# Kernel tuning notes

Measured on AMD Instinct MI355X. Metric: run time of the kernel, lower is better.

## Reference

```python
import jax, jax.numpy as jnp
import numpy as np

EMBED_DIM = 1280
NUM_HEADS = 20
HEAD_DIM = EMBED_DIM // NUM_HEADS
SEQ = 1024
BSZ = 8
ROPE_BASE = 10000.0


def _rope_cos_sin(seq_len, dim, dtype):
    # ESM RotaryEmbedding: inv_freq over even indices, emb = concat(freqs, freqs)
    inv_freq = 1.0 / (ROPE_BASE ** (jnp.arange(0, dim, 2, dtype=jnp.float32) / dim))
    t = jnp.arange(seq_len, dtype=jnp.float32)
    freqs = t[:, None] * inv_freq[None, :]          # [S, D/2]
    emb = jnp.concatenate([freqs, freqs], axis=-1)  # [S, D]
    return jnp.cos(emb).astype(dtype), jnp.sin(emb).astype(dtype)


def _rotate_half(x):
    x1, x2 = jnp.split(x, 2, axis=-1)
    return jnp.concatenate([-x2, x1], axis=-1)


def _apply_rotary(x, cos, sin):
    # x: [B, H, S, D]; cos/sin: [S, D] broadcast over B, H
    return x * cos[None, None, :, :] + _rotate_half(x) * sin[None, None, :, :]


def setup_inputs() -> dict:
    key = jax.random.key(0)
    ks = jax.random.split(key, 9)
    s = 0.02
    return {
        "query": jax.random.normal(ks[0], (SEQ, BSZ, EMBED_DIM), jnp.float32),
        "q_w": jax.random.normal(ks[1], (EMBED_DIM, EMBED_DIM), jnp.float32) * s,
        "q_b": jax.random.normal(ks[2], (EMBED_DIM,), jnp.float32) * s,
        "k_w": jax.random.normal(ks[3], (EMBED_DIM, EMBED_DIM), jnp.float32) * s,
        "k_b": jax.random.normal(ks[4], (EMBED_DIM,), jnp.float32) * s,
        "v_w": jax.random.normal(ks[5], (EMBED_DIM, EMBED_DIM), jnp.float32) * s,
        "v_b": jax.random.normal(ks[6], (EMBED_DIM,), jnp.float32) * s,
        "out_w": jax.random.normal(ks[7], (EMBED_DIM, EMBED_DIM), jnp.float32) * s,
        "out_b": jax.random.normal(ks[8], (EMBED_DIM,), jnp.float32) * s,
    }


def reference(query, q_w, q_b, k_w, k_b, v_w, v_b, out_w, out_b):
    T, B, E = query.shape
    H, D = NUM_HEADS, HEAD_DIM
    scaling = D ** -0.5

    # Separate Q/K/V projections (self-attention: key = value = query)
    q = query @ q_w.T + q_b
    k = query @ k_w.T + k_b
    v = query @ v_w.T + v_b

    # [T, B, E] -> [B, H, T, D]
    def split_heads(x):
        return x.reshape(T, B, H, D).transpose(1, 2, 0, 3)

    q, k, v = split_heads(q), split_heads(k), split_heads(v)

    # Rotary embeddings on q, k
    cos, sin = _rope_cos_sin(T, D, q.dtype)
    q = _apply_rotary(q, cos, sin)
    k = _apply_rotary(k, cos, sin)

    # SDPA with explicit scale = head_dim^-0.5
    scores = jnp.einsum("bhtd,bhsd->bhts", q, k) * scaling
    probs = jax.nn.softmax(scores, axis=-1)
    attn = jnp.einsum("bhts,bhsd->bhtd", probs, v)  # [B, H, T, D]

    # [B, H, T, D] -> [T, B, E]
    attn = attn.transpose(2, 0, 1, 3).reshape(T, B, E)
    return attn @ out_w.T + out_b
```

## Files before the change

### kernel.cpp

```cpp
#include <hip/hip_runtime.h>
#include <math.h>

#define T_SEQ 1024
#define BSZ   8
#define EMB   1280
#define NH    20
#define HD    64
#define MROWS 8192
#define KBYTES (EMB * 2)

typedef __attribute__((ext_vector_type(8))) short bf16x8;
typedef __attribute__((ext_vector_type(4))) float f32x4;

__device__ __forceinline__ short f2bf(float f) {
    unsigned u = __float_as_uint(f);
    u += 0x7fff + ((u >> 16) & 1);
    return (short)(u >> 16);
}
__device__ __forceinline__ float bf2f(short s) {
    return __uint_as_float(((unsigned)(unsigned short)s) << 16);
}

__device__ __forceinline__ void gld16(const void* g, void* l) {
    __builtin_amdgcn_global_load_lds(
        (const __attribute__((address_space(1))) void*)g,
        (__attribute__((address_space(3))) void*)l, 16, 0, 0);
}

__global__ __launch_bounds__(256) void f2bf_kernel(
    const float* __restrict__ in, short* __restrict__ out, int n8)
{
    int i = blockIdx.x * 256 + threadIdx.x;
    if (i >= n8) return;
    const float4* p = (const float4*)in;
    float4 x = p[2 * i], y = p[2 * i + 1];
    bf16x8 o;
    o[0] = f2bf(x.x); o[1] = f2bf(x.y); o[2] = f2bf(x.z); o[3] = f2bf(x.w);
    o[4] = f2bf(y.x); o[5] = f2bf(y.y); o[6] = f2bf(y.z); o[7] = f2bf(y.w);
    ((bf16x8*)out)[i] = o;
}

__global__ __launch_bounds__(256) void wcast_kernel(
    const float* __restrict__ w0, const float* __restrict__ w1,
    const float* __restrict__ w2, const float* __restrict__ w3,
    short* __restrict__ o0, short* __restrict__ o1,
    short* __restrict__ o2, short* __restrict__ o3, int n8)
{
    int which = blockIdx.y;
    const float* in = (which == 0) ? w0 : (which == 1) ? w1 : (which == 2) ? w2 : w3;
    short* out      = (which == 0) ? o0 : (which == 1) ? o1 : (which == 2) ? o2 : o3;
    int i = blockIdx.x * 256 + threadIdx.x;
    if (i >= n8) return;
    const float4* p = (const float4*)in;
    float4 x = p[2 * i], y = p[2 * i + 1];
    bf16x8 o;
    o[0] = f2bf(x.x); o[1] = f2bf(x.y); o[2] = f2bf(x.z); o[3] = f2bf(x.w);
    o[4] = f2bf(y.x); o[5] = f2bf(y.y); o[6] = f2bf(y.z); o[7] = f2bf(y.w);
    ((bf16x8*)out)[i] = o;
}

__global__ void rope_table_kernel(float* __restrict__ cost, float* __restrict__ sint) {
    int idx = blockIdx.x * 256 + threadIdx.x;
    if (idx >= T_SEQ * 32) return;
    int i = idx & 31, t = idx >> 5;
    float inv = powf(10000.0f, -(float)i / 32.0f);
    float f = (float)t * inv;
    cost[idx] = cosf(f);
    sint[idx] = sinf(f);
}

__device__ __forceinline__ void gemm_core(
    const short* __restrict__ A, const short* __restrict__ B,
    char* As, char* Bs, int m0, int n0, int tid, f32x4 (&acc)[4][4])
{
    const int l   = tid & 63;
    const int wid = tid >> 6;
    const int wr  = wid >> 1, wc = wid & 1;

    const int srow = l >> 3;
    const int scol = ((l & 7) ^ srow) << 4;
    const int g16  = (l >> 4) << 4;
    const int swx  = (l & 7) << 4;

    for (int k0 = 0; k0 < EMB; k0 += 64) {
        __syncthreads();
        #pragma unroll
        for (int c = 0; c < 4; ++c) {
            int ch  = wid * 4 + c;
            int row = ch * 8 + srow;
            gld16((const char*)A + (size_t)(m0 + row) * KBYTES + k0 * 2 + scol,
                  As + ch * 1024);
            gld16((const char*)B + (size_t)(n0 + row) * KBYTES + k0 * 2 + scol,
                  Bs + ch * 1024);
        }
        __syncthreads();
        #pragma unroll
        for (int kk = 0; kk < 2; ++kk) {
            const int cb = (kk * 64 + g16) ^ swx;
            bf16x8 af[4], bfr[4];
            #pragma unroll
            for (int m = 0; m < 4; ++m)
                af[m] = *(const bf16x8*)(As + (wr * 64 + m * 16 + (l & 15)) * 128 + cb);
            #pragma unroll
            for (int n = 0; n < 4; ++n)
                bfr[n] = *(const bf16x8*)(Bs + (wc * 64 + n * 16 + (l & 15)) * 128 + cb);
            #pragma unroll
            for (int m = 0; m < 4; ++m)
                #pragma unroll
                for (int n = 0; n < 4; ++n)
                    acc[m][n] = __builtin_amdgcn_mfma_f32_16x16x32_bf16(
                        af[m], bfr[n], acc[m][n], 0, 0, 0);
        }
    }
}

__global__ __launch_bounds__(256) void qkv_gemm_kernel(
    const short* __restrict__ A,
    const short* __restrict__ B0, const short* __restrict__ B1, const short* __restrict__ B2,
    const float* __restrict__ bias0, const float* __restrict__ bias1, const float* __restrict__ bias2,
    const float* __restrict__ cost, const float* __restrict__ sint,
    short* __restrict__ O0, short* __restrict__ O1, short* __restrict__ O2)
{
    __shared__ short As_s[8192];
    __shared__ short Bs_s[8192];

    const int z = blockIdx.z;
    const short* B = (z == 0) ? B0 : (z == 1) ? B1 : B2;
    const float* bias = (z == 0) ? bias0 : (z == 1) ? bias1 : bias2;
    short* O = (z == 0) ? O0 : (z == 1) ? O1 : O2;
    const float scale = (z == 0) ? 0.125f : 1.0f;

    const int tid = threadIdx.x;
    const int l = tid & 63;
    const int wid = tid >> 6;
    const int wr = wid >> 1, wc = wid & 1;
    const int m0 = blockIdx.x * 128;
    const int n0 = blockIdx.y * 128;

    f32x4 acc[4][4];
    const f32x4 z4 = {0.f, 0.f, 0.f, 0.f};
    #pragma unroll
    for (int m = 0; m < 4; ++m)
        #pragma unroll
        for (int n = 0; n < 4; ++n) acc[m][n] = z4;

    gemm_core(A, B, (char*)As_s, (char*)Bs_s, m0, n0, tid, acc);

    #pragma unroll
    for (int n = 0; n < 4; ++n) {
        int col = n0 + wc * 64 + n * 16 + (l & 15);
        float bv = bias[col];
        #pragma unroll
        for (int m = 0; m < 4; ++m)
            #pragma unroll
            for (int r = 0; r < 4; ++r) acc[m][n][r] += bv;
    }

    if (z < 2) {
        #pragma unroll
        for (int m = 0; m < 4; ++m) {
            #pragma unroll
            for (int r = 0; r < 4; ++r) {
                int row = m0 + wr * 64 + m * 16 + (l >> 4) * 4 + r;
                int t = row >> 3;
                #pragma unroll
                for (int n = 0; n < 2; ++n) {
                    int i = n * 16 + (l & 15);
                    float c = cost[t * 32 + i];
                    float s = sint[t * 32 + i];
                    float x1 = acc[m][n][r], x2 = acc[m][n + 2][r];
                    acc[m][n][r]     = x1 * c - x2 * s;
                    acc[m][n + 2][r] = x2 * c + x1 * s;
                }
            }
        }
    }

    #pragma unroll
    for (int n = 0; n < 4; ++n) {
        int col = n0 + wc * 64 + n * 16 + (l & 15);
        int h = col >> 6, d = col & 63;
        #pragma unroll
        for (int m = 0; m < 4; ++m) {
            #pragma unroll
            for (int r = 0; r < 4; ++r) {
                int row = m0 + wr * 64 + m * 16 + (l >> 4) * 4 + r;
                int t = row >> 3, b = row & 7;
                O[((size_t)(b * NH + h) * T_SEQ + t) * HD + d] = f2bf(acc[m][n][r] * scale);
            }
        }
    }
}

__global__ __launch_bounds__(256) void out_gemm_kernel(
    const short* __restrict__ A, const short* __restrict__ B,
    const float* __restrict__ bias, float* __restrict__ O)
{
    __shared__ short As_s[8192];
    __shared__ short Bs_s[8192];

    const int tid = threadIdx.x;
    const int l = tid & 63;
    const int wid = tid >> 6;
    const int wr = wid >> 1, wc = wid & 1;
    const int m0 = blockIdx.x * 128;
    const int n0 = blockIdx.y * 128;

    f32x4 acc[4][4];
    const f32x4 z4 = {0.f, 0.f, 0.f, 0.f};
    #pragma unroll
    for (int m = 0; m < 4; ++m)
        #pragma unroll
        for (int n = 0; n < 4; ++n) acc[m][n] = z4;

    gemm_core(A, B, (char*)As_s, (char*)Bs_s, m0, n0, tid, acc);

    #pragma unroll
    for (int n = 0; n < 4; ++n) {
        int col = n0 + wc * 64 + n * 16 + (l & 15);
        float bv = bias[col];
        #pragma unroll
        for (int m = 0; m < 4; ++m) {
            #pragma unroll
            for (int r = 0; r < 4; ++r) {
                int row = m0 + wr * 64 + m * 16 + (l >> 4) * 4 + r;
                O[(size_t)row * EMB + col] = acc[m][n][r] + bv;
            }
        }
    }
}

__global__ __launch_bounds__(256) void transpose_v_kernel(
    const short* __restrict__ v, short* __restrict__ vt)
{
    __shared__ short tv[64][72];
    const int tid = threadIdx.x;
    const int bh = blockIdx.y, t0 = blockIdx.x * 64;
    const short* src = v + ((size_t)bh * T_SEQ + t0) * HD;
    #pragma unroll
    for (int p = 0; p < 2; ++p) {
        int row = p * 32 + (tid >> 3);
        int c8 = (tid & 7) * 8;
        *(bf16x8*)&tv[row][c8] = *(const bf16x8*)(src + row * HD + c8);
    }
    __syncthreads();
    short* dst = vt + (size_t)bh * (HD * T_SEQ) + t0;
    #pragma unroll
    for (int p = 0; p < 2; ++p) {
        int d = p * 32 + (tid >> 3);
        int t8 = (tid & 7) * 8;
        bf16x8 o;
        #pragma unroll
        for (int j = 0; j < 8; ++j) o[j] = tv[t8 + j][d];
        *(bf16x8*)(dst + (size_t)d * T_SEQ + t8) = o;
    }
}

__global__ __launch_bounds__(256) void attn_kernel(
    const short* __restrict__ Q, const short* __restrict__ K,
    const short* __restrict__ Vt, short* __restrict__ Aout)
{
    __shared__ short Qs_s[4096];
    __shared__ short Ks_s[8192];
    __shared__ short Vs_s[8192];
    __shared__ short Ps_s[4096];
    char* Qs = (char*)Qs_s;
    char* Ks = (char*)Ks_s;
    char* Vs = (char*)Vs_s;
    char* Ps = (char*)Ps_s;

    const int tid = threadIdx.x;
    const int l = tid & 63;
    const int w = tid >> 6;

    const int bid = blockIdx.y * 16 + blockIdx.x;
    const int swz = (bid & 7) * 320 + (bid >> 3);
    const int q0 = (swz & 15) * 64;
    const int bh = swz >> 4;

    const int srow = l >> 3;
    const int scol = ((l & 7) ^ srow) << 4;
    const int g16  = (l >> 4) << 4;
    const int swx  = (l & 7) << 4;

    const short* Qg = Q + (size_t)bh * (T_SEQ * HD);
    const short* Kg = K + (size_t)bh * (T_SEQ * HD);
    const short* Vg = Vt + (size_t)bh * (HD * T_SEQ);

    #pragma unroll
    for (int c = 0; c < 2; ++c) {
        int ch = w * 2 + c;
        int row = ch * 8 + srow;
        gld16((const char*)Qg + (size_t)(q0 + row) * HD * 2 + scol, Qs + ch * 1024);
        gld16((const char*)Kg + (size_t)(row) * HD * 2 + scol, Ks + ch * 1024);
        gld16((const char*)Vg + ((size_t)row * T_SEQ) * 2 + scol, Vs + ch * 1024);
    }
    __syncthreads();

    f32x4 oacc[4];
    const f32x4 z4 = {0.f, 0.f, 0.f, 0.f};
    #pragma unroll
    for (int n = 0; n < 4; ++n) oacc[n] = z4;
    float m_i[4], l_i[4];
    #pragma unroll
    for (int r = 0; r < 4; ++r) { m_i[r] = -INFINITY; l_i[r] = 0.f; }

    int buf = 0;
    for (int kt = 0; kt < T_SEQ / 64; ++kt) {
        if (kt + 1 < T_SEQ / 64) {
            const int ob = (buf ^ 1) * 8192;
            #pragma unroll
            for (int c = 0; c < 2; ++c) {
                int ch = w * 2 + c;
                int row = ch * 8 + srow;
                gld16((const char*)Kg + (size_t)((kt + 1) * 64 + row) * HD * 2 + scol,
                      Ks + ob + ch * 1024);
                gld16((const char*)Vg + ((size_t)row * T_SEQ + (kt + 1) * 64) * 2 + scol,
                      Vs + ob + ch * 1024);
            }
        }
        const int cbuf = buf * 8192;

        f32x4 sacc[4];
        #pragma unroll
        for (int n = 0; n < 4; ++n) sacc[n] = z4;
        __builtin_amdgcn_s_setprio(1);
        #pragma unroll
        for (int kk = 0; kk < 2; ++kk) {
            const int cb = (kk * 64 + g16) ^ swx;
            bf16x8 aq = *(const bf16x8*)(Qs + (w * 16 + (l & 15)) * 128 + cb);
            #pragma unroll
            for (int n = 0; n < 4; ++n) {
                bf16x8 bk = *(const bf16x8*)(Ks + cbuf + (n * 16 + (l & 15)) * 128 + cb);
                sacc[n] = __builtin_amdgcn_mfma_f32_16x16x32_bf16(aq, bk, sacc[n], 0, 0, 0);
            }
        }
        __builtin_amdgcn_s_setprio(0);

        float corr[4];
        #pragma unroll
        for (int r = 0; r < 4; ++r) {
            float mx = fmaxf(fmaxf(sacc[0][r], sacc[1][r]), fmaxf(sacc[2][r], sacc[3][r]));
            mx = fmaxf(mx, __shfl_xor(mx, 1));
            mx = fmaxf(mx, __shfl_xor(mx, 2));
            mx = fmaxf(mx, __shfl_xor(mx, 4));
            mx = fmaxf(mx, __shfl_xor(mx, 8));
            float mn = fmaxf(m_i[r], mx);
            corr[r] = __expf(m_i[r] - mn);
            m_i[r] = mn;
            int prow = w * 16 + (l >> 4) * 4 + r;
            int pswx = (prow & 7) << 4;
            float rs = 0.f;
            #pragma unroll
            for (int n = 0; n < 4; ++n) {
                float p = __expf(sacc[n][r] - mn);
                rs += p;
                int kv = n * 16 + (l & 15);
                *(short*)(Ps + prow * 128 + ((kv * 2) ^ pswx)) = f2bf(p);
            }
            rs += __shfl_xor(rs, 1);
            rs += __shfl_xor(rs, 2);
            rs += __shfl_xor(rs, 4);
            rs += __shfl_xor(rs, 8);
            l_i[r] = l_i[r] * corr[r] + rs;
        }
        #pragma unroll
        for (int n = 0; n < 4; ++n) {
            f32x4 o = oacc[n];
            o[0] *= corr[0]; o[1] *= corr[1]; o[2] *= corr[2]; o[3] *= corr[3];
            oacc[n] = o;
        }

        __builtin_amdgcn_s_setprio(1);
        #pragma unroll
        for (int kk = 0; kk < 2; ++kk) {
            const int cb = (kk * 64 + g16) ^ swx;
            bf16x8 ap = *(const bf16x8*)(Ps + (w * 16 + (l & 15)) * 128 + cb);
            #pragma unroll
            for (int n = 0; n < 4; ++n) {
                bf16x8 bv = *(const bf16x8*)(Vs + cbuf + (n * 16 + (l & 15)) * 128 + cb);
                oacc[n] = __builtin_amdgcn_mfma_f32_16x16x32_bf16(ap, bv, oacc[n], 0, 0, 0);
            }
        }
        __builtin_amdgcn_s_setprio(0);

        __syncthreads();
        buf ^= 1;
    }

    const int b_ = bh / NH, h = bh % NH;
    #pragma unroll
    for (int n = 0; n < 4; ++n) {
        int d = h * HD + n * 16 + (l & 15);
        #pragma unroll
        for (int r = 0; r < 4; ++r) {
            int t = q0 + w * 16 + (l >> 4) * 4 + r;
            float v = oacc[n][r] / l_i[r];
            Aout[((size_t)t * BSZ + b_) * EMB + d] = f2bf(v);
        }
    }
}

extern "C" void kernel_launch(void* const* d_in, const int* in_sizes, int n_in,
                              void* d_out, int out_size, void* d_ws, size_t ws_size,
                              hipStream_t stream) {
    const float* X     = (const float*)d_in[0];
    const float* q_w   = (const float*)d_in[1];
    const float* q_b   = (const float*)d_in[2];
    const float* k_w   = (const float*)d_in[3];
    const float* k_b   = (const float*)d_in[4];
    const float* v_w   = (const float*)d_in[5];
    const float* v_b   = (const float*)d_in[6];
    const float* out_w = (const float*)d_in[7];
    const float* out_b = (const float*)d_in[8];
    float* out = (float*)d_out;

    short* ws = (short*)d_ws;
    const size_t NACT = (size_t)MROWS * EMB;
    const size_t NW   = (size_t)EMB * EMB;
    short* xb  = ws;
    short* wqb = xb + NACT;
    short* wkb = wqb + NW;
    short* wvb = wkb + NW;
    short* wob = wvb + NW;
    short* qb  = wob + NW;
    short* kb  = qb + NACT;
    short* vb  = kb + NACT;
    short* vtb = vb + NACT;
    short* ab  = vtb + NACT;
    float* cost = (float*)(ab + NACT);
    float* sint = cost + T_SEQ * 32;

    rope_table_kernel<<<dim3(128), 256, 0, stream>>>(cost, sint);
    f2bf_kernel<<<dim3(5120), 256, 0, stream>>>(X, xb, (int)(NACT / 8));
    wcast_kernel<<<dim3(800, 4), 256, 0, stream>>>(
        q_w, k_w, v_w, out_w, wqb, wkb, wvb, wob, (int)(NW / 8));

    qkv_gemm_kernel<<<dim3(MROWS / 128, EMB / 128, 3), 256, 0, stream>>>(
        xb, wqb, wkb, wvb, q_b, k_b, v_b, cost, sint, qb, kb, vb);

    transpose_v_kernel<<<dim3(T_SEQ / 64, BSZ * NH), 256, 0, stream>>>(vb, vtb);

    attn_kernel<<<dim3(T_SEQ / 64, BSZ * NH), 256, 0, stream>>>(qb, kb, vtb, ab);

    out_gemm_kernel<<<dim3(MROWS / 128, EMB / 128), 256, 0, stream>>>(
        ab, wob, out_b, out);
}
```

Measured before the change: 427.8 us.

## Compute transposed scores in attention to cut shuffles and add lazy rescaling

The attention kernel now computes S^T by swapping the MFMA operands, so each lane holds one query's scores and the row max and sum need only two cross-lane shuffles instead of per-row 4-step reductions. Q fragments are loaded into registers once and the Q shared buffer is reused as the P buffer, which reduces LDS use. P is written with packed 8-byte stores instead of scalar 2-byte stores. Online-softmax rescaling is skipped unless the max grows by more than 8, which trades a bounded exponent range for fewer multiplies and branches.

```diff
diff --git a/kernel.cpp b/kernel.cpp
--- a/kernel.cpp
+++ b/kernel.cpp
@@ -260,11 +260,9 @@
     const short* __restrict__ Q, const short* __restrict__ K,
     const short* __restrict__ Vt, short* __restrict__ Aout)
 {
-    __shared__ short Qs_s[4096];
     __shared__ short Ks_s[8192];
     __shared__ short Vs_s[8192];
     __shared__ short Ps_s[4096];
-    char* Qs = (char*)Qs_s;
     char* Ks = (char*)Ks_s;
     char* Vs = (char*)Vs_s;
     char* Ps = (char*)Ps_s;
@@ -272,6 +270,7 @@
     const int tid = threadIdx.x;
     const int l = tid & 63;
     const int w = tid >> 6;
+    const int g = l >> 4;
 
     const int bid = blockIdx.y * 16 + blockIdx.x;
     const int swz = (bid & 7) * 320 + (bid >> 3);
@@ -280,7 +279,7 @@
 
     const int srow = l >> 3;
     const int scol = ((l & 7) ^ srow) << 4;
-    const int g16  = (l >> 4) << 4;
+    const int g16  = g << 4;
     const int swx  = (l & 7) << 4;
 
     const short* Qg = Q + (size_t)bh * (T_SEQ * HD);
@@ -291,19 +290,25 @@
     for (int c = 0; c < 2; ++c) {
         int ch = w * 2 + c;
         int row = ch * 8 + srow;
-        gld16((const char*)Qg + (size_t)(q0 + row) * HD * 2 + scol, Qs + ch * 1024);
+        gld16((const char*)Qg + (size_t)(q0 + row) * HD * 2 + scol, Ps + ch * 1024);
         gld16((const char*)Kg + (size_t)(row) * HD * 2 + scol, Ks + ch * 1024);
         gld16((const char*)Vg + ((size_t)row * T_SEQ) * 2 + scol, Vs + ch * 1024);
     }
     __syncthreads();
 
+    bf16x8 qf[2];
+    #pragma unroll
+    for (int kk = 0; kk < 2; ++kk)
+        qf[kk] = *(const bf16x8*)(Ps + (w * 16 + (l & 15)) * 128 + ((kk * 64 + g16) ^ swx));
+
     f32x4 oacc[4];
     const f32x4 z4 = {0.f, 0.f, 0.f, 0.f};
     #pragma unroll
     for (int n = 0; n < 4; ++n) oacc[n] = z4;
-    float m_i[4], l_i[4];
-    #pragma unroll
-    for (int r = 0; r < 4; ++r) { m_i[r] = -INFINITY; l_i[r] = 0.f; }
+    float m_i = -INFINITY;
+    float l_i = 0.f;
+
+    const int pbase = (w * 16 + (l & 15)) * 128;
 
     int buf = 0;
     for (int kt = 0; kt < T_SEQ / 64; ++kt) {
@@ -321,61 +326,65 @@
         }
         const int cbuf = buf * 8192;
 
-        f32x4 sacc[4];
-        #pragma unroll
-        for (int n = 0; n < 4; ++n) sacc[n] = z4;
+        f32x4 sT[4];
+        #pragma unroll
+        for (int n = 0; n < 4; ++n) sT[n] = z4;
         __builtin_amdgcn_s_setprio(1);
         #pragma unroll
         for (int kk = 0; kk < 2; ++kk) {
             const int cb = (kk * 64 + g16) ^ swx;
-            bf16x8 aq = *(const bf16x8*)(Qs + (w * 16 + (l & 15)) * 128 + cb);
             #pragma unroll
             for (int n = 0; n < 4; ++n) {
-                bf16x8 bk = *(const bf16x8*)(Ks + cbuf + (n * 16 + (l & 15)) * 128 + cb);
-                sacc[n] = __builtin_amdgcn_mfma_f32_16x16x32_bf16(aq, bk, sacc[n], 0, 0, 0);
+                bf16x8 kf = *(const bf16x8*)(Ks + cbuf + (n * 16 + (l & 15)) * 128 + cb);
+                sT[n] = __builtin_amdgcn_mfma_f32_16x16x32_bf16(kf, qf[kk], sT[n], 0, 0, 0);
             }
         }
         __builtin_amdgcn_s_setprio(0);
 
-        float corr[4];
-        #pragma unroll
-        for (int r = 0; r < 4; ++r) {
-            float mx = fmaxf(fmaxf(sacc[0][r], sacc[1][r]), fmaxf(sacc[2][r], sacc[3][r]));
-            mx = fmaxf(mx, __shfl_xor(mx, 1));
-            mx = fmaxf(mx, __shfl_xor(mx, 2));
-            mx = fmaxf(mx, __shfl_xor(mx, 4));
-            mx = fmaxf(mx, __shfl_xor(mx, 8));
-            float mn = fmaxf(m_i[r], mx);
-            corr[r] = __expf(m_i[r] - mn);
-            m_i[r] = mn;
-            int prow = w * 16 + (l >> 4) * 4 + r;
-            int pswx = (prow & 7) << 4;
-            float rs = 0.f;
-            #pragma unroll
-            for (int n = 0; n < 4; ++n) {
-                float p = __expf(sacc[n][r] - mn);
-                rs += p;
-                int kv = n * 16 + (l & 15);
-                *(short*)(Ps + prow * 128 + ((kv * 2) ^ pswx)) = f2bf(p);
-            }
-            rs += __shfl_xor(rs, 1);
-            rs += __shfl_xor(rs, 2);
-            rs += __shfl_xor(rs, 4);
-            rs += __shfl_xor(rs, 8);
-            l_i[r] = l_i[r] * corr[r] + rs;
-        }
+        float pmax = fmaxf(fmaxf(sT[0][0], sT[0][1]), fmaxf(sT[0][2], sT[0][3]));
+        #pragma unroll
+        for (int n = 1; n < 4; ++n)
+            pmax = fmaxf(pmax, fmaxf(fmaxf(sT[n][0], sT[n][1]), fmaxf(sT[n][2], sT[n][3])));
+        pmax = fmaxf(pmax, __shfl_xor(pmax, 16));
+        pmax = fmaxf(pmax, __shfl_xor(pmax, 32));
+
+        if (__any(pmax > m_i + 8.0f)) {
+            float mn = fmaxf(m_i, pmax);
+            float corr = __expf(m_i - mn);
+            m_i = mn;
+            l_i *= corr;
+            #pragma unroll
+            for (int r = 0; r < 4; ++r) {
+                float cp = __shfl(corr, (l & 48) | (g * 4 + r));
+                #pragma unroll
+                for (int n = 0; n < 4; ++n) oacc[n][r] *= cp;
+            }
+        }
+
+        float lsum = 0.f;
         #pragma unroll
         for (int n = 0; n < 4; ++n) {
-            f32x4 o = oacc[n];
-            o[0] *= corr[0]; o[1] *= corr[1]; o[2] *= corr[2]; o[3] *= corr[3];
-            oacc[n] = o;
-        }
+            float p0 = __expf(sT[n][0] - m_i);
+            float p1 = __expf(sT[n][1] - m_i);
+            float p2 = __expf(sT[n][2] - m_i);
+            float p3 = __expf(sT[n][3] - m_i);
+            lsum += (p0 + p1) + (p2 + p3);
+            unsigned lo = ((unsigned)(unsigned short)f2bf(p0)) |
+                          (((unsigned)(unsigned short)f2bf(p1)) << 16);
+            unsigned hi = ((unsigned)(unsigned short)f2bf(p2)) |
+                          (((unsigned)(unsigned short)f2bf(p3)) << 16);
+            uint2 pk; pk.x = lo; pk.y = hi;
+            *(uint2*)(Ps + pbase + ((n * 32 + g * 8) ^ swx)) = pk;
+        }
+        lsum += __shfl_xor(lsum, 16);
+        lsum += __shfl_xor(lsum, 32);
+        l_i += lsum;
 
         __builtin_amdgcn_s_setprio(1);
         #pragma unroll
         for (int kk = 0; kk < 2; ++kk) {
             const int cb = (kk * 64 + g16) ^ swx;
-            bf16x8 ap = *(const bf16x8*)(Ps + (w * 16 + (l & 15)) * 128 + cb);
+            bf16x8 ap = *(const bf16x8*)(Ps + pbase + cb);
             #pragma unroll
             for (int n = 0; n < 4; ++n) {
                 bf16x8 bv = *(const bf16x8*)(Vs + cbuf + (n * 16 + (l & 15)) * 128 + cb);
@@ -388,15 +397,19 @@
         buf ^= 1;
     }
 
+    float inv = 1.0f / l_i;
+    float invp[4];
+    #pragma unroll
+    for (int r = 0; r < 4; ++r) invp[r] = __shfl(inv, (l & 48) | (g * 4 + r));
+
     const int b_ = bh / NH, h = bh % NH;
     #pragma unroll
     for (int n = 0; n < 4; ++n) {
         int d = h * HD + n * 16 + (l & 15);
         #pragma unroll
         for (int r = 0; r < 4; ++r) {
-            int t = q0 + w * 16 + (l >> 4) * 4 + r;
-            float v = oacc[n][r] / l_i[r];
-            Aout[((size_t)t * BSZ + b_) * EMB + d] = f2bf(v);
+            int t = q0 + w * 16 + g * 4 + r;
+            Aout[((size_t)t * BSZ + b_) * EMB + d] = f2bf(oacc[n][r] * invp[r]);
         }
     }
 }
```

Result: faster. 377.6 us (-11.7%).
